# Performance work log

Hardware: AMD Instinct MI355X
Metric: run time of the kernel (lower is better)

## Reference

```python
import jax, jax.numpy as jnp
import numpy as np

N_NODES = 50000
N_EDGES = 800000
D_FEAT = 96
HIDDEN = 256
OUT = 40


def setup_inputs() -> dict:
    key = jax.random.key(0)
    ks = jax.random.split(key, 10)
    features = jax.random.normal(ks[0], (N_NODES, D_FEAT), dtype=jnp.float32)
    src = jax.random.randint(ks[1], (N_EDGES,), 0, N_NODES, dtype=jnp.int32)
    dst = jax.random.randint(ks[2], (N_EDGES,), 0, N_NODES, dtype=jnp.int32)
    def lin(k, fan_in, fan_out):
        bound = 1.0 / np.sqrt(fan_in)
        kw, kb = jax.random.split(k)
        W = jax.random.uniform(kw, (fan_in, fan_out), jnp.float32, -bound, bound)
        b = jax.random.uniform(kb, (fan_out,), jnp.float32, -bound, bound)
        return W, b
    W1, b1 = lin(ks[3], 2 * D_FEAT, HIDDEN)
    W2, b2 = lin(ks[4], HIDDEN, HIDDEN)
    W3, b3 = lin(ks[5], HIDDEN, OUT)
    return {"features": features, "src": src, "dst": dst,
            "W1": W1, "b1": b1, "W2": W2, "b2": b2, "W3": W3, "b3": b3}


def reference(features, src, dst, W1, b1, W2, b2, W3, b3):
    # neighbor mean: gather src features, segment-sum into dst, divide by degree
    gathered = features[src]                                  # [E, D]
    summed = jax.ops.segment_sum(gathered, dst, num_segments=N_NODES)  # [N, D]
    deg = jax.ops.segment_sum(jnp.ones((N_EDGES,), jnp.float32), dst,
                              num_segments=N_NODES)           # [N]
    neighbor_feats = summed / jnp.maximum(deg, 1.0)[:, None]  # zero where no neighbors
    combined = jnp.concatenate([features, neighbor_feats], axis=1)  # [N, 2D]
    x = jax.nn.relu(combined @ W1 + b1)
    x = jax.nn.relu(x @ W2 + b2)
    return x @ W3 + b3
```

## Files before the change

kernel.cpp:

```cpp
#include <hip/hip_runtime.h>

#define N_NODES 50000
#define N_EDGES 800000
#define DF      96
#define HID     256
#define OUTF    40
#define BM      64
#define NPART   256
#define PCAP    4096

#define EPB     2048
#define NBE     ((N_EDGES + EPB - 1) / EPB)
#define CS      48

#define FEAT_THREADS (N_NODES * DF / 8)
#define FEAT_BLKS ((FEAT_THREADS + 255) / 256)
#define WSHUF_ELEMS ((96 + 128 + 24) * 512)
#define WSHUF_BLKS (WSHUF_ELEMS / 256)

typedef __attribute__((ext_vector_type(8))) short bf16x8;
typedef __attribute__((ext_vector_type(4))) float f32x4;

static __device__ __forceinline__ unsigned short f2bf(float f) {
    unsigned int u = __float_as_uint(f);
    u += 0x7fffu + ((u >> 16) & 1u);
    return (unsigned short)(u >> 16);
}
static __device__ __forceinline__ int part_of(int d) { return (d * NPART) / N_NODES; }
static __device__ __forceinline__ int part_n0(int p) { return (p * N_NODES + NPART - 1) >> 8; }

__global__ __launch_bounds__(256) void k1_prep_bin(
    const float* __restrict__ feat, const float* __restrict__ W1,
    const float* __restrict__ W2, const float* __restrict__ W3,
    const int* __restrict__ src, const int* __restrict__ dst,
    uint4* __restrict__ featbf, unsigned short* __restrict__ W1s,
    unsigned short* __restrict__ W2s, unsigned short* __restrict__ W3s,
    unsigned int* __restrict__ packed2, int* __restrict__ cellCnt)
{
    const int bid = blockIdx.x, t = threadIdx.x;
    if (bid < FEAT_BLKS) {
        int i = bid * 256 + t;
        if (i < FEAT_THREADS) {
            const float4* p = reinterpret_cast<const float4*>(feat) + (size_t)i * 2;
            float4 v0 = p[0], v1 = p[1];
            uint4 pk;
            pk.x = (unsigned)f2bf(v0.x) | ((unsigned)f2bf(v0.y) << 16);
            pk.y = (unsigned)f2bf(v0.z) | ((unsigned)f2bf(v0.w) << 16);
            pk.z = (unsigned)f2bf(v1.x) | ((unsigned)f2bf(v1.y) << 16);
            pk.w = (unsigned)f2bf(v1.z) | ((unsigned)f2bf(v1.w) << 16);
            featbf[i] = pk;
        }
        return;
    }
    if (bid < FEAT_BLKS + WSHUF_BLKS) {
        int i = (bid - FEAT_BLKS) * 256 + t;
        int j  = i & 7;
        int l  = (i >> 3) & 63;
        int fi = i >> 9;
        int kg = l >> 4, n16 = l & 15;
        if (fi < 96) {
            int tt = fi / 6, s = fi % 6;
            int k = s * 32 + kg * 8 + j, n = tt * 16 + n16;
            W1s[i] = f2bf(W1[(size_t)k * HID + n]);
        } else if (fi < 96 + 128) {
            int f2 = fi - 96;
            int tt = f2 / 8, s = f2 % 8;
            int k = s * 32 + kg * 8 + j, n = tt * 16 + n16;
            W2s[i - 96 * 512] = f2bf(W2[(size_t)k * HID + n]);
        } else {
            int f3 = fi - 224;
            int tt = f3 / 8, s = f3 % 8;
            int k = s * 32 + kg * 8 + j, n = tt * 16 + n16;
            W3s[i - 224 * 512] = (n < OUTF) ? f2bf(W3[(size_t)k * OUTF + n])
                                            : (unsigned short)0;
        }
        return;
    }
    {
        __shared__ int cur[NPART];
        const int bid2 = bid - FEAT_BLKS - WSHUF_BLKS;
        cur[t] = 0;
        __syncthreads();
        int pv[8], pos[8];
        unsigned pkv[8];
        bool valid[8];
#pragma unroll
        for (int k = 0; k < 8; ++k) {
            int e = bid2 * EPB + k * 256 + t;
            valid[k] = (e < N_EDGES);
            pv[k] = 0; pkv[k] = 0; pos[k] = CS;
            if (valid[k]) {
                int d = dst[e], s = src[e];
                int p = part_of(d);
                pv[k] = p;
                pkv[k] = ((unsigned)(d - part_n0(p)) << 16) | (unsigned)s;
                pos[k] = atomicAdd(&cur[p], 1);
            }
        }
        __syncthreads();
        cellCnt[t * NBE + bid2] = (cur[t] < CS) ? cur[t] : CS;
#pragma unroll
        for (int k = 0; k < 8; ++k) {
            if (valid[k] && pos[k] < CS)
                packed2[((size_t)pv[k] * NBE + bid2) * CS + pos[k]] = pkv[k];
        }
    }
}

__global__ __launch_bounds__(256) void partB(
    const unsigned int* __restrict__ packed2, const int* __restrict__ cellCnt,
    int* __restrict__ counts, int* __restrict__ offs,
    unsigned short* __restrict__ sorted16)
{
    __shared__ int hist[NPART];
    __shared__ int scanex[NPART];
    __shared__ int cur[NPART];
    __shared__ int totalSh;
    __shared__ unsigned short srcLDS[PCAP];
    const int p = blockIdx.x, t = threadIdx.x;
    const int n0 = part_n0(p), n1 = part_n0(p + 1);
    const int nl = n1 - n0;
    const unsigned int* cells = packed2 + (size_t)p * NBE * CS;
    const int* ccnt = cellCnt + (size_t)p * NBE;

    hist[t] = 0;
    __syncthreads();
    for (int c = t; c < NBE; c += 256) {
        int cnt = ccnt[c];
        const unsigned int* cp = cells + (size_t)c * CS;
        for (int i = 0; i < cnt; ++i)
            atomicAdd(&hist[cp[i] >> 16], 1);
    }
    __syncthreads();
    int v = hist[t];
    scanex[t] = v;
    __syncthreads();
    for (int off = 1; off < NPART; off <<= 1) {
        int x = (t >= off) ? scanex[t - off] : 0;
        __syncthreads();
        scanex[t] += x;
        __syncthreads();
    }
    int ex = scanex[t] - v;
    cur[t] = ex;
    if (t < nl) {
        counts[n0 + t] = v;
        offs[n0 + t] = p * PCAP + ex;
    }
    if (t == NPART - 1) totalSh = scanex[NPART - 1];
    __syncthreads();
    for (int c = t; c < NBE; c += 256) {
        int cnt = ccnt[c];
        const unsigned int* cp = cells + (size_t)c * CS;
        for (int i = 0; i < cnt; ++i) {
            unsigned pk = cp[i];
            int r = atomicAdd(&cur[pk >> 16], 1);
            srcLDS[r] = (unsigned short)(pk & 0xffffu);
        }
    }
    __syncthreads();
    const int total = totalSh;
    for (int i = t; i < total; i += 256)
        sorted16[p * PCAP + i] = srcLDS[i];
}

__global__ __launch_bounds__(256) void aggregate(
    const unsigned int* __restrict__ featbf,
    const unsigned short* __restrict__ sorted16,
    const int* __restrict__ offs, const int* __restrict__ counts,
    unsigned int* __restrict__ nbr32)
{
    int gw = (blockIdx.x * 256 + threadIdx.x) >> 6;
    int lane = threadIdx.x & 63;
    if (gw >= N_NODES) return;
    int beg = offs[gw];
    int cnt = counts[gw];
    const unsigned short* sp = sorted16 + beg;
    const bool act = (lane < 48);
    float a0 = 0.f, a1 = 0.f;
    int j = 0;
    for (; j + 8 <= cnt; j += 8) {
        unsigned u[8];
        if (act) {
#pragma unroll
            for (int q = 0; q < 8; ++q)
                u[q] = featbf[(size_t)sp[j + q] * 48 + lane];
#pragma unroll
            for (int q = 0; q < 8; ++q) {
                a0 += __uint_as_float(u[q] << 16);
                a1 += __uint_as_float(u[q] & 0xffff0000u);
            }
        }
    }
    for (; j + 2 <= cnt; j += 2) {
        if (act) {
            unsigned u0 = featbf[(size_t)sp[j] * 48 + lane];
            unsigned u1 = featbf[(size_t)sp[j + 1] * 48 + lane];
            a0 += __uint_as_float(u0 << 16) + __uint_as_float(u1 << 16);
            a1 += __uint_as_float(u0 & 0xffff0000u) + __uint_as_float(u1 & 0xffff0000u);
        }
    }
    if (j < cnt && act) {
        unsigned u0 = featbf[(size_t)sp[j] * 48 + lane];
        a0 += __uint_as_float(u0 << 16);
        a1 += __uint_as_float(u0 & 0xffff0000u);
    }
    float inv = 1.0f / fmaxf((float)cnt, 1.0f);
    if (act)
        nbr32[(size_t)gw * 48 + lane] =
            (unsigned)f2bf(a0 * inv) | ((unsigned)f2bf(a1 * inv) << 16);
}

__global__ __launch_bounds__(256, 2) void mlp3(
    const unsigned int* __restrict__ featbf, const unsigned int* __restrict__ nbr32,
    const unsigned short* __restrict__ W1s, const float* __restrict__ b1,
    const unsigned short* __restrict__ W2s, const float* __restrict__ b2,
    const unsigned short* __restrict__ W3s, const float* __restrict__ b3,
    float* __restrict__ out)
{
    __shared__ __align__(16) char bufA[BM * 512];
    __shared__ __align__(16) char bufB[BM * 512];

    const int t = threadIdx.x;
    const int lane = t & 63;
    const int w = t >> 6;
    const int row0 = blockIdx.x * BM;
    const int n16 = lane & 15;
    const int kg = lane >> 4;

    for (int i = t; i < BM * 24; i += 256) {
        int row = i / 24, c = i % 24;
        int half = (c >= 12) ? 1 : 0;
        int cg = c - half * 12;
        int grow = row0 + row;
        int lds_byte = (row * 384 + half * 192 + cg * 16) ^ ((row & 7) << 4);
        uint4 v = make_uint4(0u, 0u, 0u, 0u);
        if (grow < N_NODES) {
            const unsigned int* s = half ? nbr32 : featbf;
            v = *reinterpret_cast<const uint4*>(s + (size_t)grow * 48 + cg * 4);
        }
        *reinterpret_cast<uint4*>(bufA + lds_byte) = v;
    }
    __syncthreads();

    {
        f32x4 acc[4][4];
#pragma unroll
        for (int tt = 0; tt < 4; ++tt) {
            float bb = b1[(w * 4 + tt) * 16 + n16];
#pragma unroll
            for (int mt = 0; mt < 4; ++mt) {
                acc[mt][tt][0] = bb; acc[mt][tt][1] = bb;
                acc[mt][tt][2] = bb; acc[mt][tt][3] = bb;
            }
        }
#pragma unroll
        for (int s = 0; s < 6; ++s) {
            bf16x8 a[4], b[4];
#pragma unroll
            for (int mt = 0; mt < 4; ++mt) {
                int m = mt * 16 + n16;
                int byte_ = (m * 384 + s * 64 + kg * 16) ^ ((m & 7) << 4);
                a[mt] = *reinterpret_cast<const bf16x8*>(bufA + byte_);
            }
#pragma unroll
            for (int tt = 0; tt < 4; ++tt)
                b[tt] = *reinterpret_cast<const bf16x8*>(
                    W1s + ((size_t)((w * 4 + tt) * 6 + s) * 64 + lane) * 8);
#pragma unroll
            for (int mt = 0; mt < 4; ++mt)
#pragma unroll
                for (int tt = 0; tt < 4; ++tt)
                    acc[mt][tt] = __builtin_amdgcn_mfma_f32_16x16x32_bf16(
                        a[mt], b[tt], acc[mt][tt], 0, 0, 0);
        }
#pragma unroll
        for (int mt = 0; mt < 4; ++mt)
#pragma unroll
            for (int tt = 0; tt < 4; ++tt) {
                int col = (w * 4 + tt) * 16 + n16;
#pragma unroll
                for (int r = 0; r < 4; ++r) {
                    int row = mt * 16 + kg * 4 + r;
                    int byte_ = (row * 512 + col * 2) ^ ((row & 7) << 4);
                    *reinterpret_cast<unsigned short*>(bufB + byte_) =
                        f2bf(fmaxf(acc[mt][tt][r], 0.f));
                }
            }
    }
    __syncthreads();

    {
        f32x4 acc[4][4];
#pragma unroll
        for (int tt = 0; tt < 4; ++tt) {
            float bb = b2[(w * 4 + tt) * 16 + n16];
#pragma unroll
            for (int mt = 0; mt < 4; ++mt) {
                acc[mt][tt][0] = bb; acc[mt][tt][1] = bb;
                acc[mt][tt][2] = bb; acc[mt][tt][3] = bb;
            }
        }
#pragma unroll
        for (int s = 0; s < 8; ++s) {
            bf16x8 a[4], b[4];
#pragma unroll
            for (int mt = 0; mt < 4; ++mt) {
                int m = mt * 16 + n16;
                int byte_ = (m * 512 + s * 64 + kg * 16) ^ ((m & 7) << 4);
                a[mt] = *reinterpret_cast<const bf16x8*>(bufB + byte_);
            }
#pragma unroll
            for (int tt = 0; tt < 4; ++tt)
                b[tt] = *reinterpret_cast<const bf16x8*>(
                    W2s + ((size_t)((w * 4 + tt) * 8 + s) * 64 + lane) * 8);
#pragma unroll
            for (int mt = 0; mt < 4; ++mt)
#pragma unroll
                for (int tt = 0; tt < 4; ++tt)
                    acc[mt][tt] = __builtin_amdgcn_mfma_f32_16x16x32_bf16(
                        a[mt], b[tt], acc[mt][tt], 0, 0, 0);
        }
#pragma unroll
        for (int mt = 0; mt < 4; ++mt)
#pragma unroll
            for (int tt = 0; tt < 4; ++tt) {
                int col = (w * 4 + tt) * 16 + n16;
#pragma unroll
                for (int r = 0; r < 4; ++r) {
                    int row = mt * 16 + kg * 4 + r;
                    int byte_ = (row * 512 + col * 2) ^ ((row & 7) << 4);
                    *reinterpret_cast<unsigned short*>(bufA + byte_) =
                        f2bf(fmaxf(acc[mt][tt][r], 0.f));
                }
            }
    }
    __syncthreads();

    {
        f32x4 acc3[3];
#pragma unroll
        for (int tt = 0; tt < 3; ++tt) {
            int col = tt * 16 + n16;
            float bb = (col < OUTF) ? b3[col] : 0.f;
            acc3[tt][0] = bb; acc3[tt][1] = bb; acc3[tt][2] = bb; acc3[tt][3] = bb;
        }
#pragma unroll
        for (int s = 0; s < 8; ++s) {
            int m = w * 16 + n16;
            int byte_ = (m * 512 + s * 64 + kg * 16) ^ ((m & 7) << 4);
            bf16x8 a = *reinterpret_cast<const bf16x8*>(bufA + byte_);
#pragma unroll
            for (int tt = 0; tt < 3; ++tt) {
                bf16x8 b = *reinterpret_cast<const bf16x8*>(
                    W3s + ((size_t)(tt * 8 + s) * 64 + lane) * 8);
                acc3[tt] = __builtin_amdgcn_mfma_f32_16x16x32_bf16(
                    a, b, acc3[tt], 0, 0, 0);
            }
        }
#pragma unroll
        for (int tt = 0; tt < 3; ++tt) {
            int col = tt * 16 + n16;
            if (col < OUTF) {
#pragma unroll
                for (int r = 0; r < 4; ++r) {
                    int row = row0 + w * 16 + kg * 4 + r;
                    if (row < N_NODES)
                        out[(size_t)row * OUTF + col] = acc3[tt][r];
                }
            }
        }
    }
}

extern "C" void kernel_launch(void* const* d_in, const int* in_sizes, int n_in,
                              void* d_out, int out_size, void* d_ws, size_t ws_size,
                              hipStream_t stream)
{
    const float* feat = (const float*)d_in[0];
    const int*   src  = (const int*)d_in[1];
    const int*   dst  = (const int*)d_in[2];
    const float* W1   = (const float*)d_in[3];
    const float* b1   = (const float*)d_in[4];
    const float* W2   = (const float*)d_in[5];
    const float* b2   = (const float*)d_in[6];
    const float* W3   = (const float*)d_in[7];
    const float* b3   = (const float*)d_in[8];
    float* out = (float*)d_out;

    int* cellCnt = (int*)d_ws;
    int* counts  = cellCnt + NPART * NBE;
    int* offs    = counts + N_NODES;
    unsigned int* packed2 = (unsigned int*)(offs + N_NODES);
    unsigned short* sorted16 = (unsigned short*)(packed2 + (size_t)NPART * NBE * CS);
    unsigned int* featbf = (unsigned int*)(sorted16 + NPART * PCAP);
    unsigned int* nbr32  = featbf + (size_t)N_NODES * 48;
    unsigned short* W1s  = (unsigned short*)(nbr32 + (size_t)N_NODES * 48);
    unsigned short* W2s  = W1s + 96 * 512;
    unsigned short* W3s  = W2s + 128 * 512;

    k1_prep_bin<<<FEAT_BLKS + WSHUF_BLKS + NBE, 256, 0, stream>>>(
        feat, W1, W2, W3, src, dst,
        (uint4*)featbf, W1s, W2s, W3s, packed2, cellCnt);

    partB<<<NPART, 256, 0, stream>>>(packed2, cellCnt, counts, offs, sorted16);

    aggregate<<<(N_NODES * 64 + 255) / 256, 256, 0, stream>>>(
        featbf, sorted16, offs, counts, nbr32);

    mlp3<<<(N_NODES + BM - 1) / BM, 256, 0, stream>>>(
        featbf, nbr32, W1s, b1, W2s, b2, W3s, b3, out);
}
```

Measured before the change: 84.50 us.

## Fuse neighbor aggregation into MLP kernel, writing mean features directly to LDS

Removes the separate aggregate kernel and the nbr32 global buffer. Each wave of the MLP block now gathers and averages neighbor features for 16 of its 64 rows and writes the bf16 result straight into the swizzled LDS tile, so one launch and a global write plus read of the neighbor features disappear. In exchange, the gather runs at the MLP kernel's lower occupancy (launch bounds 256,2 with large LDS), so there is less parallelism to hide the latency of the random gathers. The gather is also serialized per wave before the matmul begins.

```diff
diff --git a/kernel.cpp b/kernel.cpp
--- a/kernel.cpp
+++ b/kernel.cpp
@@ -164,55 +164,10 @@
         sorted16[p * PCAP + i] = srcLDS[i];
 }
 
-__global__ __launch_bounds__(256) void aggregate(
+__global__ __launch_bounds__(256, 2) void mlp4(
     const unsigned int* __restrict__ featbf,
     const unsigned short* __restrict__ sorted16,
     const int* __restrict__ offs, const int* __restrict__ counts,
-    unsigned int* __restrict__ nbr32)
-{
-    int gw = (blockIdx.x * 256 + threadIdx.x) >> 6;
-    int lane = threadIdx.x & 63;
-    if (gw >= N_NODES) return;
-    int beg = offs[gw];
-    int cnt = counts[gw];
-    const unsigned short* sp = sorted16 + beg;
-    const bool act = (lane < 48);
-    float a0 = 0.f, a1 = 0.f;
-    int j = 0;
-    for (; j + 8 <= cnt; j += 8) {
-        unsigned u[8];
-        if (act) {
-#pragma unroll
-            for (int q = 0; q < 8; ++q)
-                u[q] = featbf[(size_t)sp[j + q] * 48 + lane];
-#pragma unroll
-            for (int q = 0; q < 8; ++q) {
-                a0 += __uint_as_float(u[q] << 16);
-                a1 += __uint_as_float(u[q] & 0xffff0000u);
-            }
-        }
-    }
-    for (; j + 2 <= cnt; j += 2) {
-        if (act) {
-            unsigned u0 = featbf[(size_t)sp[j] * 48 + lane];
-            unsigned u1 = featbf[(size_t)sp[j + 1] * 48 + lane];
-            a0 += __uint_as_float(u0 << 16) + __uint_as_float(u1 << 16);
-            a1 += __uint_as_float(u0 & 0xffff0000u) + __uint_as_float(u1 & 0xffff0000u);
-        }
-    }
-    if (j < cnt && act) {
-        unsigned u0 = featbf[(size_t)sp[j] * 48 + lane];
-        a0 += __uint_as_float(u0 << 16);
-        a1 += __uint_as_float(u0 & 0xffff0000u);
-    }
-    float inv = 1.0f / fmaxf((float)cnt, 1.0f);
-    if (act)
-        nbr32[(size_t)gw * 48 + lane] =
-            (unsigned)f2bf(a0 * inv) | ((unsigned)f2bf(a1 * inv) << 16);
-}
-
-__global__ __launch_bounds__(256, 2) void mlp3(
-    const unsigned int* __restrict__ featbf, const unsigned int* __restrict__ nbr32,
     const unsigned short* __restrict__ W1s, const float* __restrict__ b1,
     const unsigned short* __restrict__ W2s, const float* __restrict__ b2,
     const unsigned short* __restrict__ W3s, const float* __restrict__ b3,
@@ -228,18 +183,63 @@
     const int n16 = lane & 15;
     const int kg = lane >> 4;
 
-    for (int i = t; i < BM * 24; i += 256) {
-        int row = i / 24, c = i % 24;
-        int half = (c >= 12) ? 1 : 0;
-        int cg = c - half * 12;
+    for (int i = t; i < BM * 12; i += 256) {
+        int row = i / 12, c4 = i % 12;
         int grow = row0 + row;
-        int lds_byte = (row * 384 + half * 192 + cg * 16) ^ ((row & 7) << 4);
+        int lds_byte = (row * 384 + c4 * 16) ^ ((row & 7) << 4);
         uint4 v = make_uint4(0u, 0u, 0u, 0u);
-        if (grow < N_NODES) {
-            const unsigned int* s = half ? nbr32 : featbf;
-            v = *reinterpret_cast<const uint4*>(s + (size_t)grow * 48 + cg * 4);
-        }
+        if (grow < N_NODES)
+            v = *reinterpret_cast<const uint4*>(featbf + (size_t)grow * 48 + c4 * 4);
         *reinterpret_cast<uint4*>(bufA + lds_byte) = v;
+    }
+
+    {
+        const bool act = (lane < 48);
+        for (int i = 0; i < 16; ++i) {
+            int n = w * 16 + i;
+            int grow = row0 + n;
+            float a0 = 0.f, a1 = 0.f;
+            int cnt = 0;
+            if (grow < N_NODES) {
+                int beg = offs[grow];
+                cnt = counts[grow];
+                const unsigned short* sp = sorted16 + beg;
+                int j = 0;
+                for (; j + 8 <= cnt; j += 8) {
+                    unsigned u[8];
+                    if (act) {
+#pragma unroll
+                        for (int q = 0; q < 8; ++q)
+                            u[q] = featbf[(size_t)sp[j + q] * 48 + lane];
+#pragma unroll
+                        for (int q = 0; q < 8; ++q) {
+                            a0 += __uint_as_float(u[q] << 16);
+                            a1 += __uint_as_float(u[q] & 0xffff0000u);
+                        }
+                    }
+                }
+                for (; j + 2 <= cnt; j += 2) {
+                    if (act) {
+                        unsigned u0 = featbf[(size_t)sp[j] * 48 + lane];
+                        unsigned u1 = featbf[(size_t)sp[j + 1] * 48 + lane];
+                        a0 += __uint_as_float(u0 << 16) + __uint_as_float(u1 << 16);
+                        a1 += __uint_as_float(u0 & 0xffff0000u)
+                            + __uint_as_float(u1 & 0xffff0000u);
+                    }
+                }
+                if (j < cnt && act) {
+                    unsigned u0 = featbf[(size_t)sp[j] * 48 + lane];
+                    a0 += __uint_as_float(u0 << 16);
+                    a1 += __uint_as_float(u0 & 0xffff0000u);
+                }
+            }
+            float inv = 1.0f / fmaxf((float)cnt, 1.0f);
+            unsigned pk = (unsigned)f2bf(a0 * inv) | ((unsigned)f2bf(a1 * inv) << 16);
+            if (act) {
+                int byte_ = (n * 384 + 192 + lane * 4) ^ ((n & 7) << 4);
+                *reinterpret_cast<unsigned int*>(bufA + byte_) = pk;
+            }
+        }
     }
     __syncthreads();
 
@@ -394,8 +394,7 @@
     unsigned int* packed2 = (unsigned int*)(offs + N_NODES);
     unsigned short* sorted16 = (unsigned short*)(packed2 + (size_t)NPART * NBE * CS);
     unsigned int* featbf = (unsigned int*)(sorted16 + NPART * PCAP);
-    unsigned int* nbr32  = featbf + (size_t)N_NODES * 48;
-    unsigned short* W1s  = (unsigned short*)(nbr32 + (size_t)N_NODES * 48);
+    unsigned short* W1s  = (unsigned short*)(featbf + (size_t)N_NODES * 48);
     unsigned short* W2s  = W1s + 96 * 512;
     unsigned short* W3s  = W2s + 128 * 512;
 
@@ -405,9 +404,6 @@
 
     partB<<<NPART, 256, 0, stream>>>(packed2, cellCnt, counts, offs, sorted16);
 
-    aggregate<<<(N_NODES * 64 + 255) / 256, 256, 0, stream>>>(
-        featbf, sorted16, offs, counts, nbr32);
-
-    mlp3<<<(N_NODES + BM - 1) / BM, 256, 0, stream>>>(
-        featbf, nbr32, W1s, b1, W2s, b2, W3s, b3, out);
+    mlp4<<<(N_NODES + BM - 1) / BM, 256, 0, stream>>>(
+        featbf, sorted16, offs, counts, W1s, b1, W2s, b2, W3s, b3, out);
 }
```

Result: slower. 138.7 us (+64.1%).
